# Performance work log

Hardware: AMD Instinct MI355X
Metric: run time of the kernel (lower is better)

## Reference

```python
import jax, jax.numpy as jnp
import numpy as np

RULE = 30
NUM_STATES = 2
NUM_NEIGHBOURS = 1
N_SIZE = 1 + 2 * NUM_NEIGHBOURS  # 3
WRAP = True
ITERATIONS = 1024
THRESHOLD = 0.5


def make_lookup():
    # Ca1ReplaceRules.lookup: kernel[k] = rule // num_states**k % num_states
    table = [(RULE // (NUM_STATES ** k)) % NUM_STATES for k in range(NUM_STATES ** N_SIZE)]
    return jnp.array(table, dtype=jnp.uint8)  # [8]


def setup_inputs() -> dict:
    key = jax.random.key(0)
    x = jax.random.uniform(key, (16, 2048), dtype=jnp.float32)  # [batch, width]
    return {"input": x, "lookup": make_lookup()}


def reference(input, lookup):
    # threshold float input to uint8 states (lookup dtype is integer)
    state0 = (input >= THRESHOLD).astype(jnp.uint8)  # [B, W]

    def step(state, _):
        if WRAP:
            padded = jnp.concatenate([state[:, -1:], state, state[:, :1]], axis=1)
        else:
            padded = jnp.pad(state, ((0, 0), (1, 1)))
        # index[j] = left*1 + center*2 + right*4 (matches index_mult = 2**n)
        idx = (padded[:, :-2].astype(jnp.int32)
               + 2 * padded[:, 1:-1].astype(jnp.int32)
               + 4 * padded[:, 2:].astype(jnp.int32))  # [B, W]
        new = lookup[idx]  # gather, uint8 [B, W]
        return new, new

    _, hist = jax.lax.scan(step, state0, None, length=ITERATIONS)  # [T, B, W]
    full = jnp.concatenate([state0[None], hist], axis=0)  # [T+1, B, W]
    # torch permutes history to [batch, iterations+1, width]
    return jnp.transpose(full, (1, 0, 2))
```

## Files before the change

kernel.cpp:

```cpp
#include <hip/hip_runtime.h>
#include <cstdint>


#define B 16
#define W 2048
#define T_ITERS 1024
#define HIST (T_ITERS + 1)
#define LANES 64
#define K_STEPS 16
#define RBLKS (T_ITERS / K_STEPS)
#define ROW_I4 (W / 4)

typedef unsigned long long u64;
typedef int v4i __attribute__((ext_vector_type(4)));

__device__ __forceinline__ void store_nib_nt(v4i* o, unsigned nib) {
    v4i f;
    f.x = (int)(nib & 1u);
    f.y = (int)((nib >> 1) & 1u);
    f.z = (int)((nib >> 2) & 1u);
    f.w = (int)((nib >> 3) & 1u);
    __builtin_nontemporal_store(f, o);
}

__global__ __launch_bounds__(256) void ca_redundant(const float* __restrict__ x,
                                                    v4i* __restrict__ out) {
    __shared__ unsigned st[K_STEPS][LANES];
    __shared__ unsigned st0[LANES];

    const int blk = blockIdx.x;
    const int b = blk & (B - 1);
    const int r = blk >> 4;
    const int tid = threadIdx.x;
    const int wave = tid >> 6;
    const int l = tid & 63;

    if (wave == 0) {
        const float4* xv = (const float4*)(x + (size_t)b * W + (size_t)l * 32);
        unsigned m = 0;
        #pragma unroll
        for (int i = 0; i < 8; ++i) {
            float4 v = xv[i];
            unsigned n = (v.x >= 0.5f ? 1u : 0u) | (v.y >= 0.5f ? 2u : 0u) |
                         (v.z >= 0.5f ? 4u : 0u) | (v.w >= 0.5f ? 8u : 0u);
            m |= n << (4 * i);
        }
        if (r == 0) st0[l] = m;

        for (int g = 0; g <= r; ++g) {
            unsigned left  = __shfl(m, (l + LANES - 1) & (LANES - 1));
            unsigned right = __shfl(m, (l + 1) & (LANES - 1));
            u64 win = ((u64)(left >> 16)) | ((u64)m << 16) | ((u64)right << 48);
            if (g < r) {
                #pragma unroll
                for (int j = 0; j < K_STEPS; ++j)
                    win = (win >> 1) ^ (win | (win << 1));
                m = (unsigned)(win >> 16);
            } else {
                #pragma unroll
                for (int j = 0; j < K_STEPS; ++j) {
                    win = (win >> 1) ^ (win | (win << 1));
                    m = (unsigned)(win >> 16);
                    st[j][l] = m;
                }
            }
        }
    }
    __syncthreads();

    if (r == 0) {
        v4i* o = out + ((size_t)b * HIST) * ROW_I4;
        #pragma unroll
        for (int h = 0; h < 2; ++h) {
            int c = tid + 256 * h;
            unsigned u = st0[c >> 3];
            store_nib_nt(o + c, (u >> ((c & 7) * 4)) & 0xFu);
        }
    }
    #pragma unroll
    for (int jj = 0; jj < 4; ++jj) {
        const int j = wave * 4 + jj;
        v4i* o = out + ((size_t)b * HIST + (size_t)(r * K_STEPS + 1 + j)) * ROW_I4;
        #pragma unroll
        for (int i = 0; i < 8; ++i) {
            unsigned u = st[j][(l >> 3) + 8 * i];
            store_nib_nt(o + l + 64 * i, (u >> ((l & 7) * 4)) & 0xFu);
        }
    }
}

extern "C" void kernel_launch(void* const* d_in, const int* in_sizes, int n_in,
                              void* d_out, int out_size, void* d_ws, size_t ws_size,
                              hipStream_t stream) {
    const float* x = (const float*)d_in[0];
    ca_redundant<<<B * RBLKS, 256, 0, stream>>>(x, (v4i*)d_out);
}
```

Baseline: 29.43 us.

## Process four step-chunks per block with double-buffered LDS to cut redundant recompute

Each block now covers four 16-step chunks instead of one, which cuts the grid from 1024 to 256 blocks and reduces the redundant prefix recomputation each block performs. Wave 0 computes the next chunk into a second LDS buffer while all waves store the current chunk, with a barrier after each chunk. The cost is less parallelism (fewer blocks on a large GPU) and more serialization within each block.

New measurement: 30.60 us. +4.0%, slower.

```diff
diff --git a/kernel.cpp b/kernel.cpp
--- a/kernel.cpp
+++ b/kernel.cpp
@@ -8,7 +8,8 @@
 #define HIST (T_ITERS + 1)
 #define LANES 64
 #define K_STEPS 16
-#define RBLKS (T_ITERS / K_STEPS)
+#define SUBS 4
+#define QBLKS (T_ITERS / (K_STEPS * SUBS))
 #define ROW_I4 (W / 4)
 
 typedef unsigned long long u64;
@@ -23,21 +24,21 @@
     __builtin_nontemporal_store(f, o);
 }
 
-__global__ __launch_bounds__(256) void ca_redundant(const float* __restrict__ x,
-                                                    v4i* __restrict__ out) {
-    __shared__ unsigned st[K_STEPS][LANES];
+__global__ __launch_bounds__(256) void ca_pipe(const float* __restrict__ x,
+                                               v4i* __restrict__ out) {
+    __shared__ unsigned st[2][K_STEPS][LANES];
     __shared__ unsigned st0[LANES];
 
     const int blk = blockIdx.x;
     const int b = blk & (B - 1);
-    const int r = blk >> 4;
+    const int q = blk >> 4;
     const int tid = threadIdx.x;
     const int wave = tid >> 6;
     const int l = tid & 63;
 
+    unsigned m = 0;
     if (wave == 0) {
         const float4* xv = (const float4*)(x + (size_t)b * W + (size_t)l * 32);
-        unsigned m = 0;
         #pragma unroll
         for (int i = 0; i < 8; ++i) {
             float4 v = xv[i];
@@ -45,30 +46,32 @@
                          (v.z >= 0.5f ? 4u : 0u) | (v.w >= 0.5f ? 8u : 0u);
             m |= n << (4 * i);
         }
-        if (r == 0) st0[l] = m;
+        if (q == 0) st0[l] = m;
 
-        for (int g = 0; g <= r; ++g) {
+        for (int g = 0; g < q * SUBS; ++g) {
             unsigned left  = __shfl(m, (l + LANES - 1) & (LANES - 1));
             unsigned right = __shfl(m, (l + 1) & (LANES - 1));
             u64 win = ((u64)(left >> 16)) | ((u64)m << 16) | ((u64)right << 48);
-            if (g < r) {
-                #pragma unroll
-                for (int j = 0; j < K_STEPS; ++j)
-                    win = (win >> 1) ^ (win | (win << 1));
+            #pragma unroll
+            for (int j = 0; j < K_STEPS; ++j)
+                win = (win >> 1) ^ (win | (win << 1));
+            m = (unsigned)(win >> 16);
+        }
+        {
+            unsigned left  = __shfl(m, (l + LANES - 1) & (LANES - 1));
+            unsigned right = __shfl(m, (l + 1) & (LANES - 1));
+            u64 win = ((u64)(left >> 16)) | ((u64)m << 16) | ((u64)right << 48);
+            #pragma unroll
+            for (int j = 0; j < K_STEPS; ++j) {
+                win = (win >> 1) ^ (win | (win << 1));
                 m = (unsigned)(win >> 16);
-            } else {
-                #pragma unroll
-                for (int j = 0; j < K_STEPS; ++j) {
-                    win = (win >> 1) ^ (win | (win << 1));
-                    m = (unsigned)(win >> 16);
-                    st[j][l] = m;
-                }
+                st[0][j][l] = m;
             }
         }
     }
     __syncthreads();
 
-    if (r == 0) {
+    if (q == 0) {
         v4i* o = out + ((size_t)b * HIST) * ROW_I4;
         #pragma unroll
         for (int h = 0; h < 2; ++h) {
@@ -77,15 +80,32 @@
             store_nib_nt(o + c, (u >> ((c & 7) * 4)) & 0xFu);
         }
     }
-    #pragma unroll
-    for (int jj = 0; jj < 4; ++jj) {
-        const int j = wave * 4 + jj;
-        v4i* o = out + ((size_t)b * HIST + (size_t)(r * K_STEPS + 1 + j)) * ROW_I4;
+
+    for (int s = 0; s < SUBS; ++s) {
+        if (wave == 0 && s < SUBS - 1) {
+            unsigned left  = __shfl(m, (l + LANES - 1) & (LANES - 1));
+            unsigned right = __shfl(m, (l + 1) & (LANES - 1));
+            u64 win = ((u64)(left >> 16)) | ((u64)m << 16) | ((u64)right << 48);
+            unsigned* dst = &st[(s + 1) & 1][0][l];
+            #pragma unroll
+            for (int j = 0; j < K_STEPS; ++j) {
+                win = (win >> 1) ^ (win | (win << 1));
+                m = (unsigned)(win >> 16);
+                dst[j * LANES] = m;
+            }
+        }
+        const size_t t0 = (size_t)(q * (K_STEPS * SUBS) + s * K_STEPS + 1);
         #pragma unroll
-        for (int i = 0; i < 8; ++i) {
-            unsigned u = st[j][(l >> 3) + 8 * i];
-            store_nib_nt(o + l + 64 * i, (u >> ((l & 7) * 4)) & 0xFu);
+        for (int jj = 0; jj < 4; ++jj) {
+            const int j = wave * 4 + jj;
+            v4i* o = out + ((size_t)b * HIST + t0 + j) * ROW_I4;
+            #pragma unroll
+            for (int i = 0; i < 8; ++i) {
+                unsigned u = st[s & 1][j][(l >> 3) + 8 * i];
+                store_nib_nt(o + l + 64 * i, (u >> ((l & 7) * 4)) & 0xFu);
+            }
         }
+        __syncthreads();
     }
 }
 
@@ -93,5 +113,5 @@
                               void* d_out, int out_size, void* d_ws, size_t ws_size,
                               hipStream_t stream) {
     const float* x = (const float*)d_in[0];
-    ca_redundant<<<B * RBLKS, 256, 0, stream>>>(x, (v4i*)d_out);
+    ca_pipe<<<B * QBLKS, 256, 0, stream>>>(x, (v4i*)d_out);
 }
```

## Stagger chunks per block with double-buffered LDS to cut redundant recompute

Applied to the files above, without the earlier changes.

Instead of 1024 blocks each recomputing the automaton from step 0 up to their own 16-step chunk, 256 blocks each own four chunks spaced 256 steps apart. Wave 0 advances the state to the next chunk while all waves write out the current chunk from a double-buffered shared array. This removes most of the redundant serial recomputation, whose cost grew linearly with block index. In exchange there are fewer blocks, each doing more serial work, with an extra barrier per chunk.

Measured after the change: 30.78 us. 4.6% more time.

```diff
diff --git a/kernel.cpp b/kernel.cpp
--- a/kernel.cpp
+++ b/kernel.cpp
@@ -7,8 +7,10 @@
 #define T_ITERS 1024
 #define HIST (T_ITERS + 1)
 #define LANES 64
-#define K_STEPS 16
-#define RBLKS (T_ITERS / K_STEPS)
+#define CH 16
+#define NCH 4
+#define JSLOTS 16
+#define SPACING (JSLOTS * CH)
 #define ROW_I4 (W / 4)
 
 typedef unsigned long long u64;
@@ -23,21 +25,41 @@
     __builtin_nontemporal_store(f, o);
 }
 
-__global__ __launch_bounds__(256) void ca_redundant(const float* __restrict__ x,
-                                                    v4i* __restrict__ out) {
-    __shared__ unsigned st[K_STEPS][LANES];
+__device__ __forceinline__ unsigned chain16(unsigned m, int l, unsigned* dst) {
+    unsigned left  = __shfl(m, (l + LANES - 1) & (LANES - 1));
+    unsigned right = __shfl(m, (l + 1) & (LANES - 1));
+    u64 win = ((u64)(left >> 16)) | ((u64)m << 16) | ((u64)right << 48);
+    if (dst) {
+        #pragma unroll
+        for (int j = 0; j < CH; ++j) {
+            win = (win >> 1) ^ (win | (win << 1));
+            m = (unsigned)(win >> 16);
+            dst[j * LANES] = m;
+        }
+    } else {
+        #pragma unroll
+        for (int j = 0; j < CH; ++j)
+            win = (win >> 1) ^ (win | (win << 1));
+        m = (unsigned)(win >> 16);
+    }
+    return m;
+}
+
+__global__ __launch_bounds__(256) void ca_stagger(const float* __restrict__ x,
+                                                  v4i* __restrict__ out) {
+    __shared__ unsigned st[2][CH][LANES];
     __shared__ unsigned st0[LANES];
 
     const int blk = blockIdx.x;
     const int b = blk & (B - 1);
-    const int r = blk >> 4;
+    const int j = blk >> 4;
     const int tid = threadIdx.x;
     const int wave = tid >> 6;
     const int l = tid & 63;
 
+    unsigned m = 0;
     if (wave == 0) {
         const float4* xv = (const float4*)(x + (size_t)b * W + (size_t)l * 32);
-        unsigned m = 0;
         #pragma unroll
         for (int i = 0; i < 8; ++i) {
             float4 v = xv[i];
@@ -45,30 +67,14 @@
                          (v.z >= 0.5f ? 4u : 0u) | (v.w >= 0.5f ? 8u : 0u);
             m |= n << (4 * i);
         }
-        if (r == 0) st0[l] = m;
+        if (j == 0) st0[l] = m;
 
-        for (int g = 0; g <= r; ++g) {
-            unsigned left  = __shfl(m, (l + LANES - 1) & (LANES - 1));
-            unsigned right = __shfl(m, (l + 1) & (LANES - 1));
-            u64 win = ((u64)(left >> 16)) | ((u64)m << 16) | ((u64)right << 48);
-            if (g < r) {
-                #pragma unroll
-                for (int j = 0; j < K_STEPS; ++j)
-                    win = (win >> 1) ^ (win | (win << 1));
-                m = (unsigned)(win >> 16);
-            } else {
-                #pragma unroll
-                for (int j = 0; j < K_STEPS; ++j) {
-                    win = (win >> 1) ^ (win | (win << 1));
-                    m = (unsigned)(win >> 16);
-                    st[j][l] = m;
-                }
-            }
-        }
+        for (int g = 0; g < j; ++g) m = chain16(m, l, nullptr);
+        m = chain16(m, l, &st[0][0][l]);
     }
     __syncthreads();
 
-    if (r == 0) {
+    if (j == 0) {
         v4i* o = out + ((size_t)b * HIST) * ROW_I4;
         #pragma unroll
         for (int h = 0; h < 2; ++h) {
@@ -77,15 +83,24 @@
             store_nib_nt(o + c, (u >> ((c & 7) * 4)) & 0xFu);
         }
     }
-    #pragma unroll
-    for (int jj = 0; jj < 4; ++jj) {
-        const int j = wave * 4 + jj;
-        v4i* o = out + ((size_t)b * HIST + (size_t)(r * K_STEPS + 1 + j)) * ROW_I4;
+
+    for (int k = 0; k < NCH; ++k) {
+        if (wave == 0 && k < NCH - 1) {
+            for (int g = 0; g < JSLOTS - 1; ++g) m = chain16(m, l, nullptr);
+            m = chain16(m, l, &st[(k + 1) & 1][0][l]);
+        }
+        const size_t t0 = (size_t)(j * CH + k * SPACING + 1);
         #pragma unroll
-        for (int i = 0; i < 8; ++i) {
-            unsigned u = st[j][(l >> 3) + 8 * i];
-            store_nib_nt(o + l + 64 * i, (u >> ((l & 7) * 4)) & 0xFu);
+        for (int jj = 0; jj < 4; ++jj) {
+            const int jr = wave * 4 + jj;
+            v4i* o = out + ((size_t)b * HIST + t0 + jr) * ROW_I4;
+            #pragma unroll
+            for (int i = 0; i < 8; ++i) {
+                unsigned u = st[k & 1][jr][(l >> 3) + 8 * i];
+                store_nib_nt(o + l + 64 * i, (u >> ((l & 7) * 4)) & 0xFu);
+            }
         }
+        __syncthreads();
     }
 }
 
@@ -93,5 +108,5 @@
                               void* d_out, int out_size, void* d_ws, size_t ws_size,
                               hipStream_t stream) {
     const float* x = (const float*)d_in[0];
-    ca_redundant<<<B * RBLKS, 256, 0, stream>>>(x, (v4i*)d_out);
+    ca_stagger<<<B * JSLOTS, 256, 0, stream>>>(x, (v4i*)d_out);
 }
```
